# Optimization experiments

Measured on AMD Instinct MI355X. Metric: run time of the kernel, lower is better.

The kernel has to match this reference:

```python
import jax, jax.numpy as jnp
import numpy as np

N = 100000        # unique nodes in batch (node_num)
IN_DIM = 256
OUT_DIM = 128
E_RAND = 1_600_000  # random graph edges (avg degree 16)
B = N             # batch nodes (all nodes, each gets a self-loop edge)
SLOPE = 0.1       # leaky_relu slope_ratio


def setup_inputs() -> dict:
    key = jax.random.key(0)
    k1, k2, k3, k4, k5, k6 = jax.random.split(key, 6)
    x = jax.random.normal(k1, (N, IN_DIM), dtype=jnp.float32)
    # small weight scale keeps exp(leaky_relu(.)) in a sane range, like kaiming on unit-ish inputs
    W = jax.random.normal(k2, (OUT_DIM, IN_DIM), dtype=jnp.float32) * 0.05
    b = jax.random.normal(k3, (OUT_DIM,), dtype=jnp.float32) * 0.05
    a = jax.random.normal(k4, (2 * OUT_DIM, 1), dtype=jnp.float32) * 0.05
    src = jax.random.randint(k5, (E_RAND,), 0, N, dtype=jnp.int32)
    dst = jax.random.randint(k6, (E_RAND,), 0, N, dtype=jnp.int32)
    batch_idx = jnp.arange(B, dtype=jnp.int32)
    # append self-loop edges for every batch node (original vstacks original_node_edge)
    edges = jnp.stack([jnp.concatenate([src, batch_idx]),
                       jnp.concatenate([dst, batch_idx])], axis=1)  # [E_TOT, 2]
    return {"x": x, "W": W, "b": b, "a": a, "edges": edges, "batch_idx": batch_idx}


def reference(x, W, b, a, edges, batch_idx):
    # new_embeddings = Linear(in_dim -> out_dim)
    emb = x @ W.T + b  # [N, out_dim]
    # concat(h_src, h_dst) @ a  ==  h_src @ a[:d] + h_dst @ a[d:]
    a1 = a[:OUT_DIM, 0]
    a2 = a[OUT_DIM:, 0]
    s_src = emb @ a1  # [N]
    s_dst = emb @ a2  # [N]
    src, dst = edges[:, 0], edges[:, 1]
    logits = s_src[src] + s_dst[dst]                                 # [E]
    score = jnp.exp(jax.nn.leaky_relu(logits, negative_slope=SLOPE))  # [E]
    # sparse row-sum and aggregation fused as segment reductions over src
    row_sum = jax.ops.segment_sum(score, src, num_segments=N)        # [N]
    msgs = score[:, None] * emb[dst]                                 # [E, out_dim]
    results = jax.ops.segment_sum(msgs, src, num_segments=N)         # [N, out_dim]
    # nodes with no outgoing edges have row_sum==0; they are never gathered below
    safe_rs = jnp.where(row_sum > 0, row_sum, 1.0)
    out = results / safe_rs[:, None]
    return out[batch_idx]
```

## Files before the change

### kernel.cpp

```cpp
#include <hip/hip_runtime.h>
#include <hip/hip_fp16.h>

#define IN_DIM 256
#define OUT_DIM 128
#define SLOPE 0.1f

typedef __attribute__((ext_vector_type(8))) short short8;
typedef __attribute__((ext_vector_type(4))) float f32x4;

__device__ __forceinline__ unsigned bf16_rne(float f) {
    unsigned u = __float_as_uint(f);
    return (u + 0x7FFFu + ((u >> 16) & 1u)) >> 16;
}

__global__ __launch_bounds__(256) void wsplit_kernel(
    const float* __restrict__ W, short* __restrict__ Whi, short* __restrict__ Wlo)
{
    const int i = blockIdx.x * 256 + threadIdx.x;
    const float v = W[i];
    const unsigned hb = bf16_rne(v);
    const float hf = __uint_as_float(hb << 16);
    Whi[i] = (short)hb;
    Wlo[i] = (short)bf16_rne(v - hf);
}

__global__ __launch_bounds__(256) void gemm_rank_kernel(
    const float* __restrict__ x, const short* __restrict__ Whi_g,
    const short* __restrict__ Wlo_g, const float* __restrict__ bias,
    const float* __restrict__ a, __half* __restrict__ emb_h,
    float* __restrict__ s1, float* __restrict__ s2,
    const int* __restrict__ edges, int* __restrict__ deg,
    int* __restrict__ rank, int N, int E, int nGemm)
{
    __shared__ short lds[128 * 144];

    if ((int)blockIdx.x >= nGemm) {
        const int rb = (int)blockIdx.x - nGemm;
        const int e0 = (rb * 256 + (int)threadIdx.x) * 2;
        if (e0 + 1 < E) {
            const int4 ed = ((const int4*)edges)[e0 >> 1];
            const int r0 = atomicAdd(&deg[ed.x], 1);
            const int r1 = atomicAdd(&deg[ed.z], 1);
            *(int2*)&rank[e0] = make_int2(r0, r1);
        } else if (e0 < E) {
            const int2 ed = ((const int2*)edges)[e0];
            rank[e0] = atomicAdd(&deg[ed.x], 1);
        }
        return;
    }

    short* Ahi = lds;
    short* Alo = lds + 4096;
    short* Bhi = lds + 8192;
    short* Blo = lds + 12288;

    const int tid = threadIdx.x;
    const int l   = tid & 63;
    const int w   = tid >> 6;
    const int gm0 = blockIdx.x * 128;

    const int sm  = tid >> 1;
    const int kc0 = (tid & 1) * 2;

    f32x4 acc[2][8];
    #pragma unroll
    for (int i = 0; i < 2; ++i)
        #pragma unroll
        for (int j = 0; j < 8; ++j) acc[i][j] = (f32x4)0.f;

    float bias_v[8], av1[8], av2[8];
    #pragma unroll
    for (int nf = 0; nf < 8; ++nf) {
        const int col = nf * 16 + (l & 15);
        bias_v[nf] = bias[col];
        av1[nf]    = a[col];
        av2[nf]    = a[OUT_DIM + col];
    }

    for (int ks = 0; ks < 8; ++ks) {
        const int k0 = ks * 32;
        #pragma unroll
        for (int q = 0; q < 2; ++q) {
            const int kc = kc0 + q;
            {
                const int gm = gm0 + sm;
                float v[8];
                if (gm < N) {
                    const float4 p0 = *(const float4*)&x[(size_t)gm * IN_DIM + k0 + kc * 8];
                    const float4 p1 = *(const float4*)&x[(size_t)gm * IN_DIM + k0 + kc * 8 + 4];
                    v[0]=p0.x; v[1]=p0.y; v[2]=p0.z; v[3]=p0.w;
                    v[4]=p1.x; v[5]=p1.y; v[6]=p1.z; v[7]=p1.w;
                } else {
                    #pragma unroll
                    for (int j = 0; j < 8; ++j) v[j] = 0.f;
                }
                short8 h8, l8;
                #pragma unroll
                for (int j = 0; j < 8; ++j) {
                    unsigned hb = bf16_rne(v[j]);
                    float hf = __uint_as_float(hb << 16);
                    h8[j] = (short)hb;
                    l8[j] = (short)bf16_rne(v[j] - hf);
                }
                *(short8*)&Ahi[kc * 1024 + sm * 8] = h8;
                *(short8*)&Alo[kc * 1024 + sm * 8] = l8;
            }
            {
                const short8 h8 = *(const short8*)&Whi_g[sm * IN_DIM + k0 + kc * 8];
                const short8 l8 = *(const short8*)&Wlo_g[sm * IN_DIM + k0 + kc * 8];
                *(short8*)&Bhi[kc * 1024 + sm * 8] = h8;
                *(short8*)&Blo[kc * 1024 + sm * 8] = l8;
            }
        }
        __syncthreads();

        short8 ah[2], al[2];
        #pragma unroll
        for (int mf = 0; mf < 2; ++mf) {
            const int row = w * 32 + mf * 16 + (l & 15);
            const int off = (l >> 4) * 1024 + row * 8;
            ah[mf] = *(const short8*)&Ahi[off];
            al[mf] = *(const short8*)&Alo[off];
        }
        #pragma unroll
        for (int nf = 0; nf < 8; ++nf) {
            const int col = nf * 16 + (l & 15);
            const int off = (l >> 4) * 1024 + col * 8;
            short8 bh = *(const short8*)&Bhi[off];
            short8 bl = *(const short8*)&Blo[off];
            #pragma unroll
            for (int mf = 0; mf < 2; ++mf) {
                acc[mf][nf] = __builtin_amdgcn_mfma_f32_16x16x32_bf16(ah[mf], bh, acc[mf][nf], 0, 0, 0);
                acc[mf][nf] = __builtin_amdgcn_mfma_f32_16x16x32_bf16(al[mf], bh, acc[mf][nf], 0, 0, 0);
                acc[mf][nf] = __builtin_amdgcn_mfma_f32_16x16x32_bf16(ah[mf], bl, acc[mf][nf], 0, 0, 0);
            }
        }
        __syncthreads();
    }

    __half* hl = (__half*)lds;
    #pragma unroll
    for (int mf = 0; mf < 2; ++mf) {
        #pragma unroll
        for (int r = 0; r < 4; ++r) {
            const int lrow = w * 32 + mf * 16 + (l >> 4) * 4 + r;
            float p1 = 0.f, p2 = 0.f;
            #pragma unroll
            for (int nf = 0; nf < 8; ++nf) {
                const float e = acc[mf][nf][r] + bias_v[nf];
                p1 += e * av1[nf];
                p2 += e * av2[nf];
                hl[lrow * 144 + nf * 16 + (l & 15)] = __float2half(e);
            }
            p1 += __shfl_xor(p1, 1); p1 += __shfl_xor(p1, 2);
            p1 += __shfl_xor(p1, 4); p1 += __shfl_xor(p1, 8);
            p2 += __shfl_xor(p2, 1); p2 += __shfl_xor(p2, 2);
            p2 += __shfl_xor(p2, 4); p2 += __shfl_xor(p2, 8);
            const int gm = gm0 + lrow;
            if ((l & 15) == 0 && gm < N) { s1[gm] = p1; s2[gm] = p2; }
        }
    }
    __syncthreads();
    #pragma unroll
    for (int i = 0; i < 8; ++i) {
        const int idx = i * 256 + tid;
        const int row = idx >> 4, seg = idx & 15;
        if (gm0 + row < N) {
            const uint4 u = *(const uint4*)&hl[row * 144 + seg * 8];
            ((uint4*)emb_h)[(size_t)(gm0 + row) * 16 + seg] = u;
        }
    }
}

__global__ __launch_bounds__(256) void scan1_kernel(
    const int* __restrict__ deg, int* __restrict__ off,
    int* __restrict__ bsum, int N)
{
    __shared__ int lds[256];
    const int t = threadIdx.x;
    const int base = blockIdx.x * 1024 + t * 4;
    int v[4];
    int ts = 0;
    #pragma unroll
    for (int j = 0; j < 4; ++j) {
        v[j] = (base + j < N) ? deg[base + j] : 0;
        ts += v[j];
    }
    lds[t] = ts;
    __syncthreads();
    for (int d = 1; d < 256; d <<= 1) {
        int xv = (t >= d) ? lds[t - d] : 0;
        __syncthreads();
        lds[t] += xv;
        __syncthreads();
    }
    int run = lds[t] - ts;
    #pragma unroll
    for (int j = 0; j < 4; ++j) {
        if (base + j < N) off[base + j] = run;
        run += v[j];
    }
    if (t == 255) bsum[blockIdx.x] = lds[255];
}

__global__ __launch_bounds__(256) void scan2_kernel(int* __restrict__ bsum, int nb)
{
    __shared__ int lds[256];
    const int t = threadIdx.x;
    const int v = (t < nb) ? bsum[t] : 0;
    lds[t] = v;
    __syncthreads();
    for (int d = 1; d < 256; d <<= 1) {
        int xv = (t >= d) ? lds[t - d] : 0;
        __syncthreads();
        lds[t] += xv;
        __syncthreads();
    }
    if (t < nb) bsum[t] = lds[t] - v;
}

__global__ __launch_bounds__(256) void scan3_kernel(
    int* __restrict__ off, const int* __restrict__ bsum,
    const int* __restrict__ bidx, int* __restrict__ flag, int N, int E)
{
    const int i = blockIdx.x * 256 + threadIdx.x;
    if (i < N) {
        off[i] += bsum[i >> 10];
        if (bidx[i] != i) atomicOr(flag, 1);
    }
    if (i == 0) off[N] = E;
}

__global__ __launch_bounds__(256) void fill_kernel(
    const int* __restrict__ edges, const int* __restrict__ off,
    const int* __restrict__ rank, int* __restrict__ csr, int E)
{
    const int e0 = (blockIdx.x * 256 + threadIdx.x) * 2;
    if (e0 + 1 < E) {
        const int4 ed = ((const int4*)edges)[e0 >> 1];
        const int2 rk = *(const int2*)&rank[e0];
        csr[off[ed.x] + rk.x] = ed.y;
        csr[off[ed.z] + rk.y] = ed.w;
    } else if (e0 < E) {
        const int2 ed = ((const int2*)edges)[e0];
        csr[off[ed.x] + rank[e0]] = ed.y;
    }
}

__global__ __launch_bounds__(256) void agg_kernel(
    const int* __restrict__ off, const int* __restrict__ csr,
    const float* __restrict__ s1, const float* __restrict__ s2,
    const __half* __restrict__ emb_h, const int* __restrict__ flag,
    float* __restrict__ results, float* __restrict__ out, int N)
{
    const int wid  = (int)((blockIdx.x * 256u + threadIdx.x) >> 6);
    const int lane = threadIdx.x & 63;
    if (wid >= N) return;
    const int eg = lane >> 4;
    const int cl = lane & 15;
    const int beg = off[wid];
    const int end = off[wid + 1];
    const float s1n = s1[wid];

    const float4* __restrict__ embrow = (const float4*)emb_h;

    float av[8];
    #pragma unroll
    for (int k = 0; k < 8; ++k) av[k] = 0.f;
    float rs = 0.f;

    for (int base = beg; base < end; base += 16) {
        int dq[4];
        #pragma unroll
        for (int q = 0; q < 4; ++q) {
            const int idx = base + q * 4 + eg;
            dq[q] = (idx < end) ? csr[idx] : -1;
        }
        float scq[4];
        #pragma unroll
        for (int q = 0; q < 4; ++q) {
            if (dq[q] >= 0) {
                const float ll = s1n + s2[dq[q]];
                scq[q] = __expf(ll > 0.f ? ll : SLOPE * ll);
            } else {
                scq[q] = 0.f;
                dq[q]  = 0;
            }
        }
        float4 vq[4];
        #pragma unroll
        for (int q = 0; q < 4; ++q)
            vq[q] = embrow[(size_t)dq[q] * 16 + cl];
        #pragma unroll
        for (int q = 0; q < 4; ++q) {
            rs += scq[q];
            const __half2* hp = reinterpret_cast<const __half2*>(&vq[q]);
            #pragma unroll
            for (int k = 0; k < 4; ++k) {
                const float2 f = __half22float2(hp[k]);
                av[2 * k]     += scq[q] * f.x;
                av[2 * k + 1] += scq[q] * f.y;
            }
        }
    }

    #pragma unroll
    for (int k = 0; k < 8; ++k) {
        av[k] += __shfl_xor(av[k], 16);
        av[k] += __shfl_xor(av[k], 32);
    }
    rs += __shfl_xor(rs, 16);
    rs += __shfl_xor(rs, 32);

    const float inv = 1.f / (rs > 0.f ? rs : 1.f);
    if (eg == 0) {
        float* dbuf = (*flag == 0) ? out : results;
        float4* rp = (float4*)&dbuf[(size_t)wid * 128 + cl * 8];
        rp[0] = make_float4(av[0] * inv, av[1] * inv, av[2] * inv, av[3] * inv);
        rp[1] = make_float4(av[4] * inv, av[5] * inv, av[6] * inv, av[7] * inv);
    }
}

__global__ __launch_bounds__(256) void gather_kernel(
    const float* __restrict__ results, const int* __restrict__ bidx,
    const int* __restrict__ flag, float* __restrict__ out, int N)
{
    if (*flag == 0) return;
    const unsigned i = blockIdx.x * 256u + threadIdx.x;
    if (i >= (unsigned)N * 32u) return;
    const unsigned n = i >> 5, c = i & 31;
    ((float4*)out)[i] = ((const float4*)results)[(size_t)bidx[n] * 32 + c];
}

extern "C" void kernel_launch(void* const* d_in, const int* in_sizes, int n_in,
                              void* d_out, int out_size, void* d_ws, size_t ws_size,
                              hipStream_t stream) {
    const float* x     = (const float*)d_in[0];
    const float* W     = (const float*)d_in[1];
    const float* b     = (const float*)d_in[2];
    const float* a     = (const float*)d_in[3];
    const int*   edges = (const int*)d_in[4];
    const int*   bidx  = (const int*)d_in[5];

    const int N = in_sizes[5];
    const int E = in_sizes[4] / 2;

    float*  results = (float*)d_ws;
    __half* emb_h   = (__half*)(results + (size_t)N * OUT_DIM);
    float*  s1      = (float*)(emb_h + (size_t)N * OUT_DIM);
    float*  s2      = s1 + N;
    int*    deg     = (int*)(s2 + N);
    int*    flag    = deg + N;
    int*    off     = flag + 1;
    int*    bsum    = off + N + 1;
    int*    rank    = bsum + 256;
    int*    csr     = rank + E;
    short*  Whi     = (short*)(csr + E);
    short*  Wlo     = Whi + OUT_DIM * IN_DIM;

    hipMemsetAsync(deg, 0, (size_t)(N + 1) * sizeof(int), stream);

    wsplit_kernel<<<(OUT_DIM * IN_DIM) / 256, 256, 0, stream>>>(W, Whi, Wlo);

    const int nGemm = (N + 127) / 128;
    const int gE2   = (E / 2 + 255) / 256 + 1;
    gemm_rank_kernel<<<nGemm + gE2, 256, 0, stream>>>(
        x, Whi, Wlo, b, a, emb_h, s1, s2, edges, deg, rank, N, E, nGemm);

    const int nb = (N + 1023) / 1024;
    scan1_kernel<<<nb, 256, 0, stream>>>(deg, off, bsum, N);
    scan2_kernel<<<1, 256, 0, stream>>>(bsum, nb);
    scan3_kernel<<<(N + 255) / 256, 256, 0, stream>>>(off, bsum, bidx, flag, N, E);

    fill_kernel<<<gE2, 256, 0, stream>>>(edges, off, rank, csr, E);

    const unsigned aggThreads = (unsigned)N * 64u;
    agg_kernel<<<(aggThreads + 255u) / 256u, 256, 0, stream>>>(
        off, csr, s1, s2, emb_h, flag, results, (float*)d_out, N);

    const unsigned gatherThreads = (unsigned)N * 32u;
    gather_kernel<<<(gatherThreads + 255u) / 256u, 256, 0, stream>>>(
        results, bidx, flag, (float*)d_out, N);
}
```

Baseline: 214.4 us.

## Split rank counting from GEMM, register-prefetch GEMM tiles, widen edge kernels

Moves the degree/rank atomic counting out of the fused GEMM launch into its own kernel, so the two phases now run back to back instead of concurrently within one launch. Adds register double-buffering in the GEMM so the next k-slice of x and W is loaded from global memory while the current slice is split into bf16 hi/lo and staged into LDS. Rank and fill kernels now process four edges per thread instead of two. The costs are the lost overlap between GEMM and atomics, plus extra register pressure from the prefetch buffers.

Measured after the change: 236.0 us. 1.1x slower.

```diff
diff --git a/kernel.cpp b/kernel.cpp
--- a/kernel.cpp
+++ b/kernel.cpp
@@ -24,31 +24,13 @@
     Wlo[i] = (short)bf16_rne(v - hf);
 }
 
-__global__ __launch_bounds__(256) void gemm_rank_kernel(
+__global__ __launch_bounds__(256) void gemm_emb_kernel(
     const float* __restrict__ x, const short* __restrict__ Whi_g,
     const short* __restrict__ Wlo_g, const float* __restrict__ bias,
     const float* __restrict__ a, __half* __restrict__ emb_h,
-    float* __restrict__ s1, float* __restrict__ s2,
-    const int* __restrict__ edges, int* __restrict__ deg,
-    int* __restrict__ rank, int N, int E, int nGemm)
+    float* __restrict__ s1, float* __restrict__ s2, int N)
 {
     __shared__ short lds[128 * 144];
-
-    if ((int)blockIdx.x >= nGemm) {
-        const int rb = (int)blockIdx.x - nGemm;
-        const int e0 = (rb * 256 + (int)threadIdx.x) * 2;
-        if (e0 + 1 < E) {
-            const int4 ed = ((const int4*)edges)[e0 >> 1];
-            const int r0 = atomicAdd(&deg[ed.x], 1);
-            const int r1 = atomicAdd(&deg[ed.z], 1);
-            *(int2*)&rank[e0] = make_int2(r0, r1);
-        } else if (e0 < E) {
-            const int2 ed = ((const int2*)edges)[e0];
-            rank[e0] = atomicAdd(&deg[ed.x], 1);
-        }
-        return;
-    }
-
     short* Ahi = lds;
     short* Alo = lds + 4096;
     short* Bhi = lds + 8192;
@@ -61,6 +43,11 @@
 
     const int sm  = tid >> 1;
     const int kc0 = (tid & 1) * 2;
+    const int gm  = gm0 + sm;
+    const bool arow = (gm < N);
+    const float* __restrict__ xrow  = x + (size_t)(arow ? gm : 0) * IN_DIM;
+    const short* __restrict__ whrow = Whi_g + sm * IN_DIM;
+    const short* __restrict__ wlrow = Wlo_g + sm * IN_DIM;
 
     f32x4 acc[2][8];
     #pragma unroll
@@ -77,40 +64,66 @@
         av2[nf]    = a[OUT_DIM + col];
     }
 
+    float4 xbuf[2][2][2];
+    short8 whb[2][2], wlb[2][2];
+    #pragma unroll
+    for (int b = 0; b < 2; ++b)
+        #pragma unroll
+        for (int q = 0; q < 2; ++q) {
+            xbuf[b][q][0] = make_float4(0.f, 0.f, 0.f, 0.f);
+            xbuf[b][q][1] = make_float4(0.f, 0.f, 0.f, 0.f);
+        }
+
+    #pragma unroll
+    for (int q = 0; q < 2; ++q) {
+        const int kc = kc0 + q;
+        if (arow) {
+            xbuf[0][q][0] = *(const float4*)&xrow[kc * 8];
+            xbuf[0][q][1] = *(const float4*)&xrow[kc * 8 + 4];
+        }
+        whb[0][q] = *(const short8*)&whrow[kc * 8];
+        wlb[0][q] = *(const short8*)&wlrow[kc * 8];
+    }
+
+    #pragma unroll
     for (int ks = 0; ks < 8; ++ks) {
-        const int k0 = ks * 32;
+        const int cur = ks & 1;
+        const int nxt = cur ^ 1;
+
+        if (ks < 7) {
+            const int k0n = (ks + 1) * 32;
+            #pragma unroll
+            for (int q = 0; q < 2; ++q) {
+                const int kc = kc0 + q;
+                if (arow) {
+                    xbuf[nxt][q][0] = *(const float4*)&xrow[k0n + kc * 8];
+                    xbuf[nxt][q][1] = *(const float4*)&xrow[k0n + kc * 8 + 4];
+                }
+                whb[nxt][q] = *(const short8*)&whrow[k0n + kc * 8];
+                wlb[nxt][q] = *(const short8*)&wlrow[k0n + kc * 8];
+            }
+        }
+
         #pragma unroll
         for (int q = 0; q < 2; ++q) {
             const int kc = kc0 + q;
-            {
-                const int gm = gm0 + sm;
-                float v[8];
-                if (gm < N) {
-                    const float4 p0 = *(const float4*)&x[(size_t)gm * IN_DIM + k0 + kc * 8];
-                    const float4 p1 = *(const float4*)&x[(size_t)gm * IN_DIM + k0 + kc * 8 + 4];
-                    v[0]=p0.x; v[1]=p0.y; v[2]=p0.z; v[3]=p0.w;
-                    v[4]=p1.x; v[5]=p1.y; v[6]=p1.z; v[7]=p1.w;
-                } else {
-                    #pragma unroll
-                    for (int j = 0; j < 8; ++j) v[j] = 0.f;
-                }
-                short8 h8, l8;
-                #pragma unroll
-                for (int j = 0; j < 8; ++j) {
-                    unsigned hb = bf16_rne(v[j]);
-                    float hf = __uint_as_float(hb << 16);
-                    h8[j] = (short)hb;
-                    l8[j] = (short)bf16_rne(v[j] - hf);
-                }
-                *(short8*)&Ahi[kc * 1024 + sm * 8] = h8;
-                *(short8*)&Alo[kc * 1024 + sm * 8] = l8;
-            }
-            {
-                const short8 h8 = *(const short8*)&Whi_g[sm * IN_DIM + k0 + kc * 8];
-                const short8 l8 = *(const short8*)&Wlo_g[sm * IN_DIM + k0 + kc * 8];
-                *(short8*)&Bhi[kc * 1024 + sm * 8] = h8;
-                *(short8*)&Blo[kc * 1024 + sm * 8] = l8;
-            }
+            float v[8];
+            v[0] = xbuf[cur][q][0].x; v[1] = xbuf[cur][q][0].y;
+            v[2] = xbuf[cur][q][0].z; v[3] = xbuf[cur][q][0].w;
+            v[4] = xbuf[cur][q][1].x; v[5] = xbuf[cur][q][1].y;
+            v[6] = xbuf[cur][q][1].z; v[7] = xbuf[cur][q][1].w;
+            short8 h8, l8;
+            #pragma unroll
+            for (int j = 0; j < 8; ++j) {
+                unsigned hb = bf16_rne(v[j]);
+                float hf = __uint_as_float(hb << 16);
+                h8[j] = (short)hb;
+                l8[j] = (short)bf16_rne(v[j] - hf);
+            }
+            *(short8*)&Ahi[kc * 1024 + sm * 8] = h8;
+            *(short8*)&Alo[kc * 1024 + sm * 8] = l8;
+            *(short8*)&Bhi[kc * 1024 + sm * 8] = whb[cur][q];
+            *(short8*)&Blo[kc * 1024 + sm * 8] = wlb[cur][q];
         }
         __syncthreads();
 
@@ -156,8 +169,8 @@
             p1 += __shfl_xor(p1, 4); p1 += __shfl_xor(p1, 8);
             p2 += __shfl_xor(p2, 1); p2 += __shfl_xor(p2, 2);
             p2 += __shfl_xor(p2, 4); p2 += __shfl_xor(p2, 8);
-            const int gm = gm0 + lrow;
-            if ((l & 15) == 0 && gm < N) { s1[gm] = p1; s2[gm] = p2; }
+            const int gmr = gm0 + lrow;
+            if ((l & 15) == 0 && gmr < N) { s1[gmr] = p1; s2[gmr] = p2; }
         }
     }
     __syncthreads();
@@ -168,6 +181,27 @@
         if (gm0 + row < N) {
             const uint4 u = *(const uint4*)&hl[row * 144 + seg * 8];
             ((uint4*)emb_h)[(size_t)(gm0 + row) * 16 + seg] = u;
+        }
+    }
+}
+
+__global__ __launch_bounds__(256) void rank_kernel(
+    const int* __restrict__ edges, int* __restrict__ deg,
+    int* __restrict__ rank, int E)
+{
+    const int e0 = (blockIdx.x * 256 + threadIdx.x) * 4;
+    if (e0 + 3 < E) {
+        const int4 ea = ((const int4*)edges)[(e0 >> 1) + 0];
+        const int4 eb = ((const int4*)edges)[(e0 >> 1) + 1];
+        const int r0 = atomicAdd(&deg[ea.x], 1);
+        const int r1 = atomicAdd(&deg[ea.z], 1);
+        const int r2 = atomicAdd(&deg[eb.x], 1);
+        const int r3 = atomicAdd(&deg[eb.z], 1);
+        ((int4*)rank)[e0 >> 2] = make_int4(r0, r1, r2, r3);
+    } else if (e0 < E) {
+        for (int e = e0; e < E; ++e) {
+            const int2 ed = ((const int2*)edges)[e];
+            rank[e] = atomicAdd(&deg[ed.x], 1);
         }
     }
 }
@@ -235,15 +269,20 @@
     const int* __restrict__ edges, const int* __restrict__ off,
     const int* __restrict__ rank, int* __restrict__ csr, int E)
 {
-    const int e0 = (blockIdx.x * 256 + threadIdx.x) * 2;
-    if (e0 + 1 < E) {
-        const int4 ed = ((const int4*)edges)[e0 >> 1];
-        const int2 rk = *(const int2*)&rank[e0];
-        csr[off[ed.x] + rk.x] = ed.y;
-        csr[off[ed.z] + rk.y] = ed.w;
+    const int e0 = (blockIdx.x * 256 + threadIdx.x) * 4;
+    if (e0 + 3 < E) {
+        const int4 ea = ((const int4*)edges)[(e0 >> 1) + 0];
+        const int4 eb = ((const int4*)edges)[(e0 >> 1) + 1];
+        const int4 rk = ((const int4*)rank)[e0 >> 2];
+        csr[off[ea.x] + rk.x] = ea.y;
+        csr[off[ea.z] + rk.y] = ea.w;
+        csr[off[eb.x] + rk.z] = eb.y;
+        csr[off[eb.z] + rk.w] = eb.w;
     } else if (e0 < E) {
-        const int2 ed = ((const int2*)edges)[e0];
-        csr[off[ed.x] + rank[e0]] = ed.y;
+        for (int e = e0; e < E; ++e) {
+            const int2 ed = ((const int2*)edges)[e];
+            csr[off[ed.x] + rank[e]] = ed.y;
+        }
     }
 }
 
@@ -362,17 +401,18 @@
 
     wsplit_kernel<<<(OUT_DIM * IN_DIM) / 256, 256, 0, stream>>>(W, Whi, Wlo);
 
-    const int nGemm = (N + 127) / 128;
-    const int gE2   = (E / 2 + 255) / 256 + 1;
-    gemm_rank_kernel<<<nGemm + gE2, 256, 0, stream>>>(
-        x, Whi, Wlo, b, a, emb_h, s1, s2, edges, deg, rank, N, E, nGemm);
+    dim3 gGemm((N + 127) / 128);
+    gemm_emb_kernel<<<gGemm, 256, 0, stream>>>(x, Whi, Wlo, b, a, emb_h, s1, s2, N);
+
+    const int gE4 = (E / 4 + 255) / 256 + 1;
+    rank_kernel<<<gE4, 256, 0, stream>>>(edges, deg, rank, E);
 
     const int nb = (N + 1023) / 1024;
     scan1_kernel<<<nb, 256, 0, stream>>>(deg, off, bsum, N);
     scan2_kernel<<<1, 256, 0, stream>>>(bsum, nb);
     scan3_kernel<<<(N + 255) / 256, 256, 0, stream>>>(off, bsum, bidx, flag, N, E);
 
-    fill_kernel<<<gE2, 256, 0, stream>>>(edges, off, rank, csr, E);
+    fill_kernel<<<gE4, 256, 0, stream>>>(edges, off, rank, csr, E);
 
     const unsigned aggThreads = (unsigned)N * 64u;
     agg_kernel<<<(aggThreads + 255u) / 256u, 256, 0, stream>>>(
```

## Fold degree atomics into GEMM blocks and widen CSR fill per thread

Applied to the files above, without the earlier changes.

Instead of separate rank blocks appended to the GEMM grid, every GEMM thread now issues up to EPT degree atomics before the matrix work, holds the ranks in registers, and writes them out at the end, so atomic latency can overlap the GEMM. A tail kernel covers any edges beyond the per-thread capacity. The fill kernel now handles four edges per thread with wider loads. This costs extra registers in the GEMM kernel, which may reduce occupancy, and ties the GEMM blocks to the atomic traffic.

Result: slower. 223.9 us (+4.4%).

```diff
diff --git a/kernel.cpp b/kernel.cpp
--- a/kernel.cpp
+++ b/kernel.cpp
@@ -4,6 +4,7 @@
 #define IN_DIM 256
 #define OUT_DIM 128
 #define SLOPE 0.1f
+#define EPT 10
 
 typedef __attribute__((ext_vector_type(8))) short short8;
 typedef __attribute__((ext_vector_type(4))) float f32x4;
@@ -24,31 +25,15 @@
     Wlo[i] = (short)bf16_rne(v - hf);
 }
 
-__global__ __launch_bounds__(256) void gemm_rank_kernel(
+__global__ __launch_bounds__(256) void gemm_emb_kernel(
     const float* __restrict__ x, const short* __restrict__ Whi_g,
     const short* __restrict__ Wlo_g, const float* __restrict__ bias,
     const float* __restrict__ a, __half* __restrict__ emb_h,
     float* __restrict__ s1, float* __restrict__ s2,
     const int* __restrict__ edges, int* __restrict__ deg,
-    int* __restrict__ rank, int N, int E, int nGemm)
+    int* __restrict__ rank, int N, int E)
 {
     __shared__ short lds[128 * 144];
-
-    if ((int)blockIdx.x >= nGemm) {
-        const int rb = (int)blockIdx.x - nGemm;
-        const int e0 = (rb * 256 + (int)threadIdx.x) * 2;
-        if (e0 + 1 < E) {
-            const int4 ed = ((const int4*)edges)[e0 >> 1];
-            const int r0 = atomicAdd(&deg[ed.x], 1);
-            const int r1 = atomicAdd(&deg[ed.z], 1);
-            *(int2*)&rank[e0] = make_int2(r0, r1);
-        } else if (e0 < E) {
-            const int2 ed = ((const int2*)edges)[e0];
-            rank[e0] = atomicAdd(&deg[ed.x], 1);
-        }
-        return;
-    }
-
     short* Ahi = lds;
     short* Alo = lds + 4096;
     short* Bhi = lds + 8192;
@@ -58,6 +43,19 @@
     const int l   = tid & 63;
     const int w   = tid >> 6;
     const int gm0 = blockIdx.x * 128;
+
+    const int gtid = blockIdx.x * 256 + tid;
+    const int T    = (int)gridDim.x * 256;
+    int rnk[EPT];
+    #pragma unroll
+    for (int i = 0; i < EPT; ++i) {
+        const int e = gtid + i * T;
+        rnk[i] = 0;
+        if (e < E) {
+            const int2 ed = ((const int2*)edges)[e];
+            rnk[i] = atomicAdd(&deg[ed.x], 1);
+        }
+    }
 
     const int sm  = tid >> 1;
     const int kc0 = (tid & 1) * 2;
@@ -170,6 +168,22 @@
             ((uint4*)emb_h)[(size_t)(gm0 + row) * 16 + seg] = u;
         }
     }
+
+    #pragma unroll
+    for (int i = 0; i < EPT; ++i) {
+        const int e = gtid + i * T;
+        if (e < E) rank[e] = rnk[i];
+    }
+}
+
+__global__ __launch_bounds__(256) void rank_tail_kernel(
+    const int* __restrict__ edges, int* __restrict__ deg,
+    int* __restrict__ rank, int e0base, int E)
+{
+    const int e = e0base + blockIdx.x * 256 + threadIdx.x;
+    if (e >= E) return;
+    const int2 ed = ((const int2*)edges)[e];
+    rank[e] = atomicAdd(&deg[ed.x], 1);
 }
 
 __global__ __launch_bounds__(256) void scan1_kernel(
@@ -235,15 +249,20 @@
     const int* __restrict__ edges, const int* __restrict__ off,
     const int* __restrict__ rank, int* __restrict__ csr, int E)
 {
-    const int e0 = (blockIdx.x * 256 + threadIdx.x) * 2;
-    if (e0 + 1 < E) {
-        const int4 ed = ((const int4*)edges)[e0 >> 1];
-        const int2 rk = *(const int2*)&rank[e0];
-        csr[off[ed.x] + rk.x] = ed.y;
-        csr[off[ed.z] + rk.y] = ed.w;
+    const int e0 = (blockIdx.x * 256 + threadIdx.x) * 4;
+    if (e0 + 3 < E) {
+        const int4 ea = ((const int4*)edges)[(e0 >> 1) + 0];
+        const int4 eb = ((const int4*)edges)[(e0 >> 1) + 1];
+        const int4 rk = ((const int4*)rank)[e0 >> 2];
+        csr[off[ea.x] + rk.x] = ea.y;
+        csr[off[ea.z] + rk.y] = ea.w;
+        csr[off[eb.x] + rk.z] = eb.y;
+        csr[off[eb.z] + rk.w] = eb.w;
     } else if (e0 < E) {
-        const int2 ed = ((const int2*)edges)[e0];
-        csr[off[ed.x] + rank[e0]] = ed.y;
+        for (int e = e0; e < E; ++e) {
+            const int2 ed = ((const int2*)edges)[e];
+            csr[off[ed.x] + rank[e]] = ed.y;
+        }
     }
 }
 
@@ -363,16 +382,23 @@
     wsplit_kernel<<<(OUT_DIM * IN_DIM) / 256, 256, 0, stream>>>(W, Whi, Wlo);
 
     const int nGemm = (N + 127) / 128;
-    const int gE2   = (E / 2 + 255) / 256 + 1;
-    gemm_rank_kernel<<<nGemm + gE2, 256, 0, stream>>>(
-        x, Whi, Wlo, b, a, emb_h, s1, s2, edges, deg, rank, N, E, nGemm);
+    gemm_emb_kernel<<<nGemm, 256, 0, stream>>>(
+        x, Whi, Wlo, b, a, emb_h, s1, s2, edges, deg, rank, N, E);
+
+    const long long cap = (long long)nGemm * 256 * EPT;
+    if ((long long)E > cap) {
+        const int tailE = E - (int)cap;
+        rank_tail_kernel<<<(tailE + 255) / 256, 256, 0, stream>>>(
+            edges, deg, rank, (int)cap, E);
+    }
 
     const int nb = (N + 1023) / 1024;
     scan1_kernel<<<nb, 256, 0, stream>>>(deg, off, bsum, N);
     scan2_kernel<<<1, 256, 0, stream>>>(bsum, nb);
     scan3_kernel<<<(N + 255) / 256, 256, 0, stream>>>(off, bsum, bidx, flag, N, E);
 
-    fill_kernel<<<gE2, 256, 0, stream>>>(edges, off, rank, csr, E);
+    const int gE4 = (E / 4 + 255) / 256 + 1;
+    fill_kernel<<<gE4, 256, 0, stream>>>(edges, off, rank, csr, E);
 
     const unsigned aggThreads = (unsigned)N * 64u;
     agg_kernel<<<(aggThreads + 255u) / 256u, 256, 0, stream>>>(
```
